# Kernel optimization log

Hardware: AMD Instinct MI355X
Metric: run time of the kernel (lower is better)

## Reference

```python
import jax, jax.numpy as jnp
import numpy as np

EPS = 1e-7  # K.epsilon()
ROUTINGS = 3
NUM_CAPSULE = 8
FILTERS = 16


def squash(v, axis=-1):
    s2 = jnp.sum(jnp.square(v), axis=axis, keepdims=True)
    scale = s2 / (1.0 + s2) / jnp.sqrt(s2 + EPS)
    return scale * v


def _conv_per_caps(x, w):
    # x: [B,H,W,Cin], w: [k,k,Cin,Cout]
    return jax.lax.conv_general_dilated(
        x, w, window_strides=(1, 1), padding='SAME',
        dimension_numbers=('NHWC', 'HWIO', 'NHWC'))


def setup_inputs() -> dict:
    key = jax.random.key(0)
    k1, k2 = jax.random.split(key, 2)
    B, H, Wd, IN_CAPS, IN_F = 32, 32, 32, 8, 16
    input_tensor = jax.random.normal(k1, (B, H, Wd, IN_CAPS, IN_F), dtype=jnp.float32)
    # he_normal fan_in = k*k*Cin = 3*3*16 = 144
    W = jax.random.normal(k2, (IN_CAPS, 3, 3, IN_F, NUM_CAPSULE * FILTERS), dtype=jnp.float32) * np.sqrt(2.0 / 144.0)
    b = jnp.full((1, 1, NUM_CAPSULE, FILTERS), 0.1, dtype=jnp.float32)
    return {"input_tensor": input_tensor, "W": W, "b": b}


def reference(input_tensor, W, b):
    B, H, Wd, in_caps, in_f = input_tensor.shape
    # per-input-capsule conv: vmap over capsule axis of input and weight
    votes = jax.vmap(_conv_per_caps, in_axes=(3, 0), out_axes=1)(input_tensor, W)
    # [B, in_caps, H, W, num_cap*F] -> [B, in_caps, H, W, num_cap, F]
    votes = votes.reshape(B, in_caps, H, Wd, NUM_CAPSULE, FILTERS)

    # dynamic routing
    logits = jnp.zeros((B, in_caps, H, Wd, NUM_CAPSULE), dtype=votes.dtype)
    activation = None
    for i in range(ROUTINGS):
        route = jax.nn.softmax(logits, axis=-1)  # over output capsules
        # sum over input capsules of route-weighted votes, plus bias
        preactivate = jnp.einsum('bihwc,bihwcf->bhwcf', route, votes) + b
        activation = squash(preactivate, axis=-1)
        if i < ROUTINGS - 1:
            # scalar-product agreement
            logits = logits + jnp.einsum('bihwcf,bhwcf->bihwc', votes, activation)
    return activation.astype(jnp.float32)
```

## Files before the change

kernel.cpp:

```cpp
#include <hip/hip_runtime.h>
#include <math.h>


typedef _Float16 fp16x8 __attribute__((ext_vector_type(8)));
typedef float f32x4 __attribute__((ext_vector_type(4)));

#define EPS 1e-7f
constexpr int PSTRIDE = 136;
constexpr int PCOLS   = 34;
constexpr int LSTRIDE = 76;
constexpr int PXS     = 76;
constexpr int W_ELEMS = 40 * 8 * 64 * 8;

__device__ __forceinline__ float sumquad(float v) {
    v += __shfl_xor(v, 16);
    v += __shfl_xor(v, 32);
    return v;
}

__global__ __launch_bounds__(256)
void prep_weights(const float* __restrict__ wts,
                  _Float16* __restrict__ w16) {
    int n = blockIdx.x * 256 + threadIdx.x;
    if (n >= W_ELEMS) return;
    int j    = n & 7;
    int ln   = (n >> 3) & 63;
    int c0   = (n >> 9) & 7;
    int iq   = n >> 12;
    int i0   = iq / 5;
    int q0   = iq - i0 * 5;
    int k = q0 * 32 + (ln >> 4) * 8 + j;
    float w = 0.f;
    if (k < 144) w = wts[(i0 * 144 + k) * 128 + c0 * 16 + (ln & 15)];
    w16[n] = (_Float16)w;
}

__global__ __launch_bounds__(512, 4)
void capsule_mfma_kernel(const float* __restrict__ x,
                         const _Float16* __restrict__ w16,
                         const float* __restrict__ bias,
                         float* __restrict__ out)
{
    __shared__ _Float16 patch[3 * PCOLS * PSTRIDE];
    __shared__ float lg_arr[32 * LSTRIDE];
    __shared__ float r_arr[32 * PXS];

    const int tid  = threadIdx.x;
    const int lane = tid & 63;
    const int c    = tid >> 6;
    const int l15  = lane & 15;
    const int quad = lane >> 4;
    const int lane8 = lane * 8;

    const int bid = blockIdx.x;
    const int h = bid & 31, b = bid >> 5;

    const float4* x4 = (const float4*)x;
    for (int idx = tid; idx < 3 * PCOLS * 32; idx += 512) {
        int ch4  = idx & 31;
        int slot = idx >> 5;
        int row  = slot / PCOLS;
        int colp = slot - row * PCOLS;
        int gh = h - 1 + row;
        int gw = colp - 1;
        float4 v = {0.f, 0.f, 0.f, 0.f};
        if ((unsigned)gh < 32u && (unsigned)gw < 32u)
            v = x4[(((b * 32 + gh) * 32 + gw) << 5) + ch4];
        _Float16 ph[4];
        ph[0] = (_Float16)v.x; ph[1] = (_Float16)v.y;
        ph[2] = (_Float16)v.z; ph[3] = (_Float16)v.w;
        *(ushort4*)&patch[slot * PSTRIDE + ch4 * 4] = *(const ushort4*)ph;
    }
    __syncthreads();

    int a_off[5];
    #pragma unroll
    for (int q = 0; q < 5; ++q) {
        int tap = 2 * q + (quad >> 1);
        if (tap > 8) tap = 8;
        int dy = tap / 3, dx = tap - dy * 3;
        a_off[q] = (dy * PCOLS + l15 + dx) * PSTRIDE + (quad & 1) * 8;
    }

    f32x4 acc[2][8];
    #pragma unroll
    for (int mt = 0; mt < 2; ++mt)
        #pragma unroll
        for (int i = 0; i < 8; ++i) acc[mt][i] = (f32x4){0.f, 0.f, 0.f, 0.f};

    #pragma unroll
    for (int q = 0; q < 5; ++q) {
        #pragma unroll
        for (int i = 0; i < 8; ++i) {
            int woff = ((i * 5 + q) * 8 + c) * 512 + lane8;
            fp16x8 aw = *(const fp16x8*)(w16 + woff);
            fp16x8 b0 = *(const fp16x8*)(patch + a_off[q] + i * 16);
            fp16x8 b1 = *(const fp16x8*)(patch + a_off[q] + 16 * PSTRIDE + i * 16);
            acc[0][i] = __builtin_amdgcn_mfma_f32_16x16x32_f16(aw, b0, acc[0][i], 0, 0, 0);
            acc[1][i] = __builtin_amdgcn_mfma_f32_16x16x32_f16(aw, b1, acc[1][i], 0, 0, 0);
        }
    }

    const float4 bb4 = *(const float4*)(bias + c * 16 + quad * 4);
    const float barr[4] = {bb4.x, bb4.y, bb4.z, bb4.w};

    float actv[2][4];

    #pragma unroll
    for (int mt = 0; mt < 2; ++mt) {
        float pre[4];
        #pragma unroll
        for (int r = 0; r < 4; ++r) {
            float s = acc[mt][0][r] + acc[mt][1][r] + acc[mt][2][r] + acc[mt][3][r]
                    + acc[mt][4][r] + acc[mt][5][r] + acc[mt][6][r] + acc[mt][7][r];
            pre[r] = s * 0.125f + barr[r];
        }
        float s2 = sumquad(pre[0]*pre[0] + pre[1]*pre[1] + pre[2]*pre[2] + pre[3]*pre[3]);
        float scale = s2 * __builtin_amdgcn_rsqf(s2 + EPS) * __builtin_amdgcn_rcpf(1.f + s2);
        #pragma unroll
        for (int r = 0; r < 4; ++r) actv[mt][r] = scale * pre[r];
    }
    #pragma unroll
    for (int mt = 0; mt < 2; ++mt)
        #pragma unroll
        for (int i = 0; i < 8; ++i) {
            float t = acc[mt][i][0]*actv[mt][0] + acc[mt][i][1]*actv[mt][1]
                    + acc[mt][i][2]*actv[mt][2] + acc[mt][i][3]*actv[mt][3];
            t = sumquad(t);
            if (quad == 0) lg_arr[(mt * 16 + l15) * LSTRIDE + i * 9 + c] = t;
        }
    __syncthreads();
    if (tid < 256) {
        int p = tid >> 3, ii = tid & 7;
        const float* lrow = &lg_arr[p * LSTRIDE + ii * 9];
        float m = lrow[0];
        #pragma unroll
        for (int cc = 1; cc < 8; ++cc) m = fmaxf(m, lrow[cc]);
        float e[8]; float den = 0.f;
        #pragma unroll
        for (int cc = 0; cc < 8; ++cc) { e[cc] = __expf(lrow[cc] - m); den += e[cc]; }
        float rd = __builtin_amdgcn_rcpf(den);
        #pragma unroll
        for (int cc = 0; cc < 8; ++cc) r_arr[p * PXS + cc * 8 + ii] = e[cc] * rd;
    }
    __syncthreads();

    #pragma unroll
    for (int mt = 0; mt < 2; ++mt) {
        const float4* rp = (const float4*)&r_arr[(mt * 16 + l15) * PXS + c * 8];
        float4 r0 = rp[0], r1 = rp[1];
        float pre[4];
        #pragma unroll
        for (int r = 0; r < 4; ++r) {
            float s;
            s  = r0.x * acc[mt][0][r]; s = fmaf(r0.y, acc[mt][1][r], s);
            s  = fmaf(r0.z, acc[mt][2][r], s); s = fmaf(r0.w, acc[mt][3][r], s);
            s  = fmaf(r1.x, acc[mt][4][r], s); s = fmaf(r1.y, acc[mt][5][r], s);
            s  = fmaf(r1.z, acc[mt][6][r], s); s = fmaf(r1.w, acc[mt][7][r], s);
            pre[r] = s + barr[r];
        }
        float s2 = sumquad(pre[0]*pre[0] + pre[1]*pre[1] + pre[2]*pre[2] + pre[3]*pre[3]);
        float scale = s2 * __builtin_amdgcn_rsqf(s2 + EPS) * __builtin_amdgcn_rcpf(1.f + s2);
        #pragma unroll
        for (int r = 0; r < 4; ++r) actv[mt][r] = scale * pre[r];
    }
    #pragma unroll
    for (int mt = 0; mt < 2; ++mt)
        #pragma unroll
        for (int i = 0; i < 8; ++i) {
            float t = acc[mt][i][0]*actv[mt][0] + acc[mt][i][1]*actv[mt][1]
                    + acc[mt][i][2]*actv[mt][2] + acc[mt][i][3]*actv[mt][3];
            t = sumquad(t);
            if (quad == 0) lg_arr[(mt * 16 + l15) * LSTRIDE + i * 9 + c] += t;
        }
    __syncthreads();
    if (tid < 256) {
        int p = tid >> 3, ii = tid & 7;
        const float* lrow = &lg_arr[p * LSTRIDE + ii * 9];
        float m = lrow[0];
        #pragma unroll
        for (int cc = 1; cc < 8; ++cc) m = fmaxf(m, lrow[cc]);
        float e[8]; float den = 0.f;
        #pragma unroll
        for (int cc = 0; cc < 8; ++cc) { e[cc] = __expf(lrow[cc] - m); den += e[cc]; }
        float rd = __builtin_amdgcn_rcpf(den);
        #pragma unroll
        for (int cc = 0; cc < 8; ++cc) r_arr[p * PXS + cc * 8 + ii] = e[cc] * rd;
    }
    __syncthreads();

    #pragma unroll
    for (int mt = 0; mt < 2; ++mt) {
        const float4* rp = (const float4*)&r_arr[(mt * 16 + l15) * PXS + c * 8];
        float4 r0 = rp[0], r1 = rp[1];
        float pre[4];
        #pragma unroll
        for (int r = 0; r < 4; ++r) {
            float s;
            s  = r0.x * acc[mt][0][r]; s = fmaf(r0.y, acc[mt][1][r], s);
            s  = fmaf(r0.z, acc[mt][2][r], s); s = fmaf(r0.w, acc[mt][3][r], s);
            s  = fmaf(r1.x, acc[mt][4][r], s); s = fmaf(r1.y, acc[mt][5][r], s);
            s  = fmaf(r1.z, acc[mt][6][r], s); s = fmaf(r1.w, acc[mt][7][r], s);
            pre[r] = s + barr[r];
        }
        float s2 = sumquad(pre[0]*pre[0] + pre[1]*pre[1] + pre[2]*pre[2] + pre[3]*pre[3]);
        float scale = s2 * __builtin_amdgcn_rsqf(s2 + EPS) * __builtin_amdgcn_rcpf(1.f + s2);
        float4 o4 = { scale*pre[0], scale*pre[1], scale*pre[2], scale*pre[3] };
        int px = mt * 16 + l15;
        *(float4*)(out + (((b * 32 + h) * 32 + px) << 7) + c * 16 + quad * 4) = o4;
    }
}

extern "C" void kernel_launch(void* const* d_in, const int* in_sizes, int n_in,
                              void* d_out, int out_size, void* d_ws, size_t ws_size,
                              hipStream_t stream) {
    const float* x    = (const float*)d_in[0];
    const float* wts  = (const float*)d_in[1];
    const float* bias = (const float*)d_in[2];
    float* out        = (float*)d_out;
    _Float16* w16     = (_Float16*)d_ws;

    prep_weights<<<dim3(640), dim3(256), 0, stream>>>(wts, w16);
    capsule_mfma_kernel<<<dim3(1024), dim3(512), 0, stream>>>(x, w16, bias, out);
}
```

Before: 102.7 us.

## Split fused conv+routing kernel into separate conv and routing kernels via workspace

The single fused kernel is split into a conv kernel that writes the MFMA vote accumulators to a workspace buffer and a routing kernel that reloads them and runs the dynamic routing. This may be aimed at profiling each stage or at lowering per-kernel register and LDS pressure. In exchange it adds a global round trip of the full votes tensor, about 64 MB written and read, plus an extra launch.

New measurement: 133.5 us. +30.0%, slower.

```diff
diff --git a/kernel.cpp b/kernel.cpp
--- a/kernel.cpp
+++ b/kernel.cpp
@@ -11,6 +11,7 @@
 constexpr int LSTRIDE = 76;
 constexpr int PXS     = 76;
 constexpr int W_ELEMS = 40 * 8 * 64 * 8;
+constexpr size_t VOTES_OFF = 524288;
 
 __device__ __forceinline__ float sumquad(float v) {
     v += __shfl_xor(v, 16);
@@ -36,14 +37,11 @@
 }
 
 __global__ __launch_bounds__(512, 4)
-void capsule_mfma_kernel(const float* __restrict__ x,
-                         const _Float16* __restrict__ w16,
-                         const float* __restrict__ bias,
-                         float* __restrict__ out)
+void conv_votes_kernel(const float* __restrict__ x,
+                       const _Float16* __restrict__ w16,
+                       float4* __restrict__ votes4)
 {
     __shared__ _Float16 patch[3 * PCOLS * PSTRIDE];
-    __shared__ float lg_arr[32 * LSTRIDE];
-    __shared__ float r_arr[32 * PXS];
 
     const int tid  = threadIdx.x;
     const int lane = tid & 63;
@@ -101,6 +99,41 @@
         }
     }
 
+    const int gw = bid * 8 + c;
+    #pragma unroll
+    for (int mt = 0; mt < 2; ++mt)
+        #pragma unroll
+        for (int i = 0; i < 8; ++i)
+            votes4[(gw * 16 + mt * 8 + i) * 64 + lane] = *(const float4*)&acc[mt][i];
+}
+
+__global__ __launch_bounds__(512, 4)
+void routing_kernel(const float4* __restrict__ votes4,
+                    const float* __restrict__ bias,
+                    float* __restrict__ out)
+{
+    __shared__ float lg_arr[32 * LSTRIDE];
+    __shared__ float r_arr[32 * PXS];
+
+    const int tid  = threadIdx.x;
+    const int lane = tid & 63;
+    const int c    = tid >> 6;
+    const int l15  = lane & 15;
+    const int quad = lane >> 4;
+
+    const int bid = blockIdx.x;
+    const int h = bid & 31, b = bid >> 5;
+    const int gw = bid * 8 + c;
+
+    f32x4 acc[2][8];
+    #pragma unroll
+    for (int mt = 0; mt < 2; ++mt)
+        #pragma unroll
+        for (int i = 0; i < 8; ++i) {
+            float4 v = votes4[(gw * 16 + mt * 8 + i) * 64 + lane];
+            acc[mt][i] = (f32x4){v.x, v.y, v.z, v.w};
+        }
+
     const float4 bb4 = *(const float4*)(bias + c * 16 + quad * 4);
     const float barr[4] = {bb4.x, bb4.y, bb4.z, bb4.w};
 
@@ -219,7 +252,9 @@
     const float* bias = (const float*)d_in[2];
     float* out        = (float*)d_out;
     _Float16* w16     = (_Float16*)d_ws;
+    float4* votes4    = (float4*)((char*)d_ws + VOTES_OFF);
 
     prep_weights<<<dim3(640), dim3(256), 0, stream>>>(wts, w16);
-    capsule_mfma_kernel<<<dim3(1024), dim3(512), 0, stream>>>(x, w16, bias, out);
-}
+    conv_votes_kernel<<<dim3(1024), dim3(512), 0, stream>>>(x, w16, votes4);
+    routing_kernel<<<dim3(1024), dim3(512), 0, stream>>>(votes4, bias, out);
+}
```

## Pre-convert input to padded fp16 buffer and read MFMA operands from global

Applied to the files above, without the earlier changes.

Adds a separate kernel that converts the input to fp16 and writes it into a zero-padded 34x34 layout in the workspace. The main kernel no longer stages a shared-memory patch; MFMA B operands are loaded straight from the padded global buffer, which removes the in-kernel conversion loop and a barrier. The cost is an extra launch, an extra round trip through global memory for the converted input, and repeated global/L2 reads of overlapping rows in place of LDS reuse.

Result: slower. 161.5 us (+57.3%).

```diff
diff --git a/kernel.cpp b/kernel.cpp
--- a/kernel.cpp
+++ b/kernel.cpp
@@ -6,11 +6,11 @@
 typedef float f32x4 __attribute__((ext_vector_type(4)));
 
 #define EPS 1e-7f
-constexpr int PSTRIDE = 136;
-constexpr int PCOLS   = 34;
 constexpr int LSTRIDE = 76;
 constexpr int PXS     = 76;
 constexpr int W_ELEMS = 40 * 8 * 64 * 8;
+constexpr size_t X16P_OFF = 524288;
+constexpr int XP_CHUNKS = 32 * 34 * 34 * 16;
 
 __device__ __forceinline__ float sumquad(float v) {
     v += __shfl_xor(v, 16);
@@ -35,13 +35,37 @@
     w16[n] = (_Float16)w;
 }
 
+__global__ __launch_bounds__(256)
+void prep_x16(const float* __restrict__ x, _Float16* __restrict__ x16p) {
+    int n8 = blockIdx.x * 256 + threadIdx.x;
+    int chunk = n8 & 15;
+    int rest  = n8 >> 4;
+    int gw    = rest % 34;
+    int rest2 = rest / 34;
+    int gh    = rest2 % 34;
+    int b     = rest2 / 34;
+    _Float16 h8[8];
+    if ((unsigned)(gh - 1) < 32u && (unsigned)(gw - 1) < 32u) {
+        const float4* xs = (const float4*)x
+            + ((((b * 32 + gh - 1) * 32) + gw - 1) << 5) + chunk * 2;
+        float4 v0 = xs[0], v1 = xs[1];
+        h8[0] = (_Float16)v0.x; h8[1] = (_Float16)v0.y;
+        h8[2] = (_Float16)v0.z; h8[3] = (_Float16)v0.w;
+        h8[4] = (_Float16)v1.x; h8[5] = (_Float16)v1.y;
+        h8[6] = (_Float16)v1.z; h8[7] = (_Float16)v1.w;
+    } else {
+        #pragma unroll
+        for (int t = 0; t < 8; ++t) h8[t] = (_Float16)0.f;
+    }
+    *(uint4*)(x16p + (size_t)n8 * 8) = *(const uint4*)h8;
+}
+
 __global__ __launch_bounds__(512, 4)
-void capsule_mfma_kernel(const float* __restrict__ x,
+void capsule_mfma_kernel(const _Float16* __restrict__ x16p,
                          const _Float16* __restrict__ w16,
                          const float* __restrict__ bias,
                          float* __restrict__ out)
 {
-    __shared__ _Float16 patch[3 * PCOLS * PSTRIDE];
     __shared__ float lg_arr[32 * LSTRIDE];
     __shared__ float r_arr[32 * PXS];
 
@@ -55,31 +79,16 @@
     const int bid = blockIdx.x;
     const int h = bid & 31, b = bid >> 5;
 
-    const float4* x4 = (const float4*)x;
-    for (int idx = tid; idx < 3 * PCOLS * 32; idx += 512) {
-        int ch4  = idx & 31;
-        int slot = idx >> 5;
-        int row  = slot / PCOLS;
-        int colp = slot - row * PCOLS;
-        int gh = h - 1 + row;
-        int gw = colp - 1;
-        float4 v = {0.f, 0.f, 0.f, 0.f};
-        if ((unsigned)gh < 32u && (unsigned)gw < 32u)
-            v = x4[(((b * 32 + gh) * 32 + gw) << 5) + ch4];
-        _Float16 ph[4];
-        ph[0] = (_Float16)v.x; ph[1] = (_Float16)v.y;
-        ph[2] = (_Float16)v.z; ph[3] = (_Float16)v.w;
-        *(ushort4*)&patch[slot * PSTRIDE + ch4 * 4] = *(const ushort4*)ph;
-    }
-    __syncthreads();
-
-    int a_off[5];
+    const _Float16* xb = x16p + (size_t)b * (34 * 34 * 128);
+    int boff0[5], boff1[5];
     #pragma unroll
     for (int q = 0; q < 5; ++q) {
         int tap = 2 * q + (quad >> 1);
         if (tap > 8) tap = 8;
         int dy = tap / 3, dx = tap - dy * 3;
-        a_off[q] = (dy * PCOLS + l15 + dx) * PSTRIDE + (quad & 1) * 8;
+        int rowbase = (h + dy) * (34 * 128);
+        boff0[q] = rowbase + (l15 + dx) * 128 + (quad & 1) * 8;
+        boff1[q] = rowbase + (16 + l15 + dx) * 128 + (quad & 1) * 8;
     }
 
     f32x4 acc[2][8];
@@ -94,8 +103,8 @@
         for (int i = 0; i < 8; ++i) {
             int woff = ((i * 5 + q) * 8 + c) * 512 + lane8;
             fp16x8 aw = *(const fp16x8*)(w16 + woff);
-            fp16x8 b0 = *(const fp16x8*)(patch + a_off[q] + i * 16);
-            fp16x8 b1 = *(const fp16x8*)(patch + a_off[q] + 16 * PSTRIDE + i * 16);
+            fp16x8 b0 = *(const fp16x8*)(xb + boff0[q] + i * 16);
+            fp16x8 b1 = *(const fp16x8*)(xb + boff1[q] + i * 16);
             acc[0][i] = __builtin_amdgcn_mfma_f32_16x16x32_f16(aw, b0, acc[0][i], 0, 0, 0);
             acc[1][i] = __builtin_amdgcn_mfma_f32_16x16x32_f16(aw, b1, acc[1][i], 0, 0, 0);
         }
@@ -219,7 +228,9 @@
     const float* bias = (const float*)d_in[2];
     float* out        = (float*)d_out;
     _Float16* w16     = (_Float16*)d_ws;
+    _Float16* x16p    = (_Float16*)((char*)d_ws + X16P_OFF);
 
     prep_weights<<<dim3(640), dim3(256), 0, stream>>>(wts, w16);
-    capsule_mfma_kernel<<<dim3(1024), dim3(512), 0, stream>>>(x, w16, bias, out);
-}
+    prep_x16<<<dim3(XP_CHUNKS / 256), dim3(256), 0, stream>>>(x, x16p);
+    capsule_mfma_kernel<<<dim3(1024), dim3(512), 0, stream>>>(x16p, w16, bias, out);
+}
```

## Process two output rows per block to share halo patch loads

Applied to the files above, without the earlier changes.

Each block now handles two adjacent output rows with 1024 threads (two groups of 8 waves) instead of one row with 512 threads. The staged input patch grows from 3 to 4 rows, so the halo-row loads and fp16 conversion are shared between the two rows, cutting redundant global reads of x from 3x to 2x per row. Grid size halves to 512 blocks. The cost is larger LDS use and 1024-thread blocks, which may reduce how many blocks fit per CU and weaken latency hiding. The `__launch_bounds__(1024, 4)` hint also asks for more resident waves than before, which may limit registers for the 64 accumulator floats.

Measured after the change: 102.0 us (median of 2 runs). Within noise of the previous version (-0.7%).

```diff
diff --git a/kernel.cpp b/kernel.cpp
--- a/kernel.cpp
+++ b/kernel.cpp
@@ -8,6 +8,7 @@
 #define EPS 1e-7f
 constexpr int PSTRIDE = 136;
 constexpr int PCOLS   = 34;
+constexpr int PROWS   = 4;
 constexpr int LSTRIDE = 76;
 constexpr int PXS     = 76;
 constexpr int W_ELEMS = 40 * 8 * 64 * 8;
@@ -35,28 +36,31 @@
     w16[n] = (_Float16)w;
 }
 
-__global__ __launch_bounds__(512, 4)
+__global__ __launch_bounds__(1024, 4)
 void capsule_mfma_kernel(const float* __restrict__ x,
                          const _Float16* __restrict__ w16,
                          const float* __restrict__ bias,
                          float* __restrict__ out)
 {
-    __shared__ _Float16 patch[3 * PCOLS * PSTRIDE];
-    __shared__ float lg_arr[32 * LSTRIDE];
-    __shared__ float r_arr[32 * PXS];
+    __shared__ _Float16 patch[PROWS * PCOLS * PSTRIDE];
+    __shared__ float lg_arr[64 * LSTRIDE];
+    __shared__ float r_arr[64 * PXS];
 
     const int tid  = threadIdx.x;
     const int lane = tid & 63;
-    const int c    = tid >> 6;
+    const int w    = tid >> 6;
+    const int c    = w & 7;
+    const int g    = w >> 3;
     const int l15  = lane & 15;
     const int quad = lane >> 4;
     const int lane8 = lane * 8;
 
     const int bid = blockIdx.x;
-    const int h = bid & 31, b = bid >> 5;
+    const int h2 = bid & 15, b = bid >> 4;
+    const int h = h2 << 1;
 
     const float4* x4 = (const float4*)x;
-    for (int idx = tid; idx < 3 * PCOLS * 32; idx += 512) {
+    for (int idx = tid; idx < PROWS * PCOLS * 32; idx += 1024) {
         int ch4  = idx & 31;
         int slot = idx >> 5;
         int row  = slot / PCOLS;
@@ -79,7 +83,7 @@
         int tap = 2 * q + (quad >> 1);
         if (tap > 8) tap = 8;
         int dy = tap / 3, dx = tap - dy * 3;
-        a_off[q] = (dy * PCOLS + l15 + dx) * PSTRIDE + (quad & 1) * 8;
+        a_off[q] = ((g + dy) * PCOLS + l15 + dx) * PSTRIDE + (quad & 1) * 8;
     }
 
     f32x4 acc[2][8];
@@ -121,16 +125,18 @@
         for (int r = 0; r < 4; ++r) actv[mt][r] = scale * pre[r];
     }
     #pragma unroll
-    for (int mt = 0; mt < 2; ++mt)
+    for (int mt = 0; mt < 2; ++mt) {
+        int slot = g * 32 + mt * 16 + l15;
         #pragma unroll
         for (int i = 0; i < 8; ++i) {
             float t = acc[mt][i][0]*actv[mt][0] + acc[mt][i][1]*actv[mt][1]
                     + acc[mt][i][2]*actv[mt][2] + acc[mt][i][3]*actv[mt][3];
             t = sumquad(t);
-            if (quad == 0) lg_arr[(mt * 16 + l15) * LSTRIDE + i * 9 + c] = t;
-        }
-    __syncthreads();
-    if (tid < 256) {
+            if (quad == 0) lg_arr[slot * LSTRIDE + i * 9 + c] = t;
+        }
+    }
+    __syncthreads();
+    if (tid < 512) {
         int p = tid >> 3, ii = tid & 7;
         const float* lrow = &lg_arr[p * LSTRIDE + ii * 9];
         float m = lrow[0];
@@ -147,7 +153,8 @@
 
     #pragma unroll
     for (int mt = 0; mt < 2; ++mt) {
-        const float4* rp = (const float4*)&r_arr[(mt * 16 + l15) * PXS + c * 8];
+        int slot = g * 32 + mt * 16 + l15;
+        const float4* rp = (const float4*)&r_arr[slot * PXS + c * 8];
         float4 r0 = rp[0], r1 = rp[1];
         float pre[4];
         #pragma unroll
@@ -165,16 +172,18 @@
         for (int r = 0; r < 4; ++r) actv[mt][r] = scale * pre[r];
     }
     #pragma unroll
-    for (int mt = 0; mt < 2; ++mt)
+    for (int mt = 0; mt < 2; ++mt) {
+        int slot = g * 32 + mt * 16 + l15;
         #pragma unroll
         for (int i = 0; i < 8; ++i) {
             float t = acc[mt][i][0]*actv[mt][0] + acc[mt][i][1]*actv[mt][1]
                     + acc[mt][i][2]*actv[mt][2] + acc[mt][i][3]*actv[mt][3];
             t = sumquad(t);
-            if (quad == 0) lg_arr[(mt * 16 + l15) * LSTRIDE + i * 9 + c] += t;
-        }
-    __syncthreads();
-    if (tid < 256) {
+            if (quad == 0) lg_arr[slot * LSTRIDE + i * 9 + c] += t;
+        }
+    }
+    __syncthreads();
+    if (tid < 512) {
         int p = tid >> 3, ii = tid & 7;
         const float* lrow = &lg_arr[p * LSTRIDE + ii * 9];
         float m = lrow[0];
@@ -191,7 +200,8 @@
 
     #pragma unroll
     for (int mt = 0; mt < 2; ++mt) {
-        const float4* rp = (const float4*)&r_arr[(mt * 16 + l15) * PXS + c * 8];
+        int slot = g * 32 + mt * 16 + l15;
+        const float4* rp = (const float4*)&r_arr[slot * PXS + c * 8];
         float4 r0 = rp[0], r1 = rp[1];
         float pre[4];
         #pragma unroll
@@ -206,8 +216,9 @@
         float s2 = sumquad(pre[0]*pre[0] + pre[1]*pre[1] + pre[2]*pre[2] + pre[3]*pre[3]);
         float scale = s2 * __builtin_amdgcn_rsqf(s2 + EPS) * __builtin_amdgcn_rcpf(1.f + s2);
         float4 o4 = { scale*pre[0], scale*pre[1], scale*pre[2], scale*pre[3] };
+        int gh = h + g;
         int px = mt * 16 + l15;
-        *(float4*)(out + (((b * 32 + h) * 32 + px) << 7) + c * 16 + quad * 4) = o4;
+        *(float4*)(out + (((b * 32 + gh) * 32 + px) << 7) + c * 16 + quad * 4) = o4;
     }
 }
 
@@ -221,5 +232,5 @@
     _Float16* w16     = (_Float16*)d_ws;
 
     prep_weights<<<dim3(640), dim3(256), 0, stream>>>(wts, w16);
-    capsule_mfma_kernel<<<dim3(1024), dim3(512), 0, stream>>>(x, w16, bias, out);
-}
+    capsule_mfma_kernel<<<dim3(512), dim3(1024), 0, stream>>>(x, w16, bias, out);
+}
```
